# Performance work log

Hardware: AMD Instinct MI355X
Metric: run time of the kernel (lower is better)

Reference implementation:

```python
import jax, jax.numpy as jnp
import numpy as np

N_EMBD = 1024
N_HEAD = 16
HEAD_DIM = N_EMBD // N_HEAD
EPS = 1e-5


def setup_inputs() -> dict:
    key = jax.random.key(0)
    ks = jax.random.split(key, 12)
    C = N_EMBD
    s = lambda fan_in: 1.0 / np.sqrt(fan_in)
    return {
        "x": jax.random.normal(ks[0], (2, 2048, C), dtype=jnp.float32),
        "ln1_g": jnp.ones((C,), jnp.float32),
        "ln1_b": jnp.zeros((C,), jnp.float32),
        "w_attn": jax.random.normal(ks[1], (C, 3 * C), jnp.float32) * s(C),
        "b_attn": jnp.zeros((3 * C,), jnp.float32),
        "w_proj": jax.random.normal(ks[2], (C, C), jnp.float32) * s(C),
        "b_proj": jnp.zeros((C,), jnp.float32),
        "ln2_g": jnp.ones((C,), jnp.float32),
        "ln2_b": jnp.zeros((C,), jnp.float32),
        "w_fc": jax.random.normal(ks[3], (C, 4 * C), jnp.float32) * s(C),
        "b_fc": jnp.zeros((4 * C,), jnp.float32),
        "w_fc2": jax.random.normal(ks[4], (4 * C, C), jnp.float32) * s(4 * C),
        "b_fc2": jnp.zeros((C,), jnp.float32),
    }


def _layernorm(x, g, b):
    mu = jnp.mean(x, axis=-1, keepdims=True)
    var = jnp.mean(jnp.square(x - mu), axis=-1, keepdims=True)
    return (x - mu) * jax.lax.rsqrt(var + EPS) * g + b


def _attention(x, w_attn, b_attn, w_proj, b_proj):
    B, T, C = x.shape
    qkv = x @ w_attn + b_attn  # [B,T,3C]
    q, k, v = jnp.split(qkv, 3, axis=-1)
    # [B,H,T,D]
    reshape = lambda t: t.reshape(B, T, N_HEAD, HEAD_DIM).transpose(0, 2, 1, 3)
    q, k, v = reshape(q), reshape(k), reshape(v)
    scale = HEAD_DIM ** (-0.5)
    att = jnp.einsum("bhqd,bhkd->bhqk", q, k) * scale  # [B,H,T,T]
    mask = jnp.tril(jnp.ones((T, T), dtype=bool))
    att = jnp.where(mask, att, -jnp.inf)
    att = jax.nn.softmax(att, axis=-1)
    y = jnp.einsum("bhqk,bhkd->bhqd", att, v)
    y = y.transpose(0, 2, 1, 3).reshape(B, T, C)
    return y @ w_proj + b_proj


def _mlp(x, w_fc, b_fc, w_fc2, b_fc2):
    h = jax.nn.gelu(x @ w_fc + b_fc, approximate=False)  # nn.GELU default = exact erf
    return h @ w_fc2 + b_fc2


def reference(x, ln1_g, ln1_b, w_attn, b_attn, w_proj, b_proj,
              ln2_g, ln2_b, w_fc, b_fc, w_fc2, b_fc2):
    x = x + _attention(_layernorm(x, ln1_g, ln1_b), w_attn, b_attn, w_proj, b_proj)
    x = x + _mlp(_layernorm(x, ln2_g, ln2_b), w_fc, b_fc, w_fc2, b_fc2)
    return x
```

## Files before the change

kernel.cpp:

```cpp
#include <hip/hip_runtime.h>
#include <hip/hip_bf16.h>
#include <math.h>

typedef __attribute__((ext_vector_type(8))) __bf16 bf16x8;
typedef __attribute__((ext_vector_type(4))) float floatx4;
typedef __attribute__((ext_vector_type(8))) unsigned short ushort8;

#define C_EMBD 1024
#define T_SEQ 2048
#define NH 16
#define HD 64

static __device__ __forceinline__ unsigned short f2b(float f) {
  __hip_bfloat16 h = __float2bfloat16(f);
  unsigned short u;
  __builtin_memcpy(&u, &h, sizeof(u));
  return u;
}
static __device__ __forceinline__ float b2f(unsigned short u) {
  unsigned int b = ((unsigned int)u) << 16;
  float f;
  __builtin_memcpy(&f, &b, sizeof(f));
  return f;
}

static __device__ __forceinline__ void gload16(const void* g, void* l) {
  __builtin_amdgcn_global_load_lds(
      (__attribute__((address_space(1))) void*)(void*)g,
      (__attribute__((address_space(3))) void*)l, 16, 0, 0);
}

static __device__ __forceinline__ floatx4 mfma_bf16(bf16x8 a, bf16x8 b, floatx4 c) {
  return __builtin_amdgcn_mfma_f32_16x16x32_bf16(a, b, c, 0, 0, 0);
}

__global__ __launch_bounds__(256) void wtrans(const float* __restrict__ in,
                                              unsigned short* __restrict__ out,
                                              int K, int N) {
  __shared__ float t[32][33];
  int n0 = blockIdx.x * 32, k0 = blockIdx.y * 32;
  int tx = threadIdx.x & 31, ty = threadIdx.x >> 5;
#pragma unroll
  for (int i = 0; i < 4; i++)
    t[ty + i * 8][tx] = in[(size_t)(k0 + ty + i * 8) * N + n0 + tx];
  __syncthreads();
#pragma unroll
  for (int i = 0; i < 4; i++)
    out[(size_t)(n0 + ty + i * 8) * K + k0 + tx] = f2b(t[tx][ty + i * 8]);
}

__global__ __launch_bounds__(256) void ln_fwd(const float* __restrict__ x,
                                              const float* __restrict__ g,
                                              const float* __restrict__ bta,
                                              unsigned short* __restrict__ out) {
  int row = blockIdx.x;
  int t = threadIdx.x;
  const float4* xr = (const float4*)(x + (size_t)row * C_EMBD);
  float4 v = xr[t];
  float s = v.x + v.y + v.z + v.w;
  float ss = v.x * v.x + v.y * v.y + v.z * v.z + v.w * v.w;
#pragma unroll
  for (int m = 1; m < 64; m <<= 1) {
    s += __shfl_xor(s, m, 64);
    ss += __shfl_xor(ss, m, 64);
  }
  __shared__ float ps[8];
  int wv = t >> 6;
  if ((t & 63) == 0) { ps[wv] = s; ps[4 + wv] = ss; }
  __syncthreads();
  s = ps[0] + ps[1] + ps[2] + ps[3];
  ss = ps[4] + ps[5] + ps[6] + ps[7];
  float mu = s * (1.0f / C_EMBD);
  float var = ss * (1.0f / C_EMBD) - mu * mu;
  float rs = rsqrtf(var + 1e-5f);
  float4 gv = ((const float4*)g)[t];
  float4 bv = ((const float4*)bta)[t];
  ushort4 o;
  o.x = f2b((v.x - mu) * rs * gv.x + bv.x);
  o.y = f2b((v.y - mu) * rs * gv.y + bv.y);
  o.z = f2b((v.z - mu) * rs * gv.z + bv.z);
  o.w = f2b((v.w - mu) * rs * gv.w + bv.w);
  *(ushort4*)(out + (size_t)row * C_EMBD + t * 4) = o;
}

template <int EP, int MI>
__global__ __launch_bounds__(256) void gemm_bt(const unsigned short* __restrict__ A,
                                               const unsigned short* __restrict__ Bt,
                                               const float* __restrict__ bias,
                                               const float* __restrict__ res,
                                               void* __restrict__ outv,
                                               unsigned short* __restrict__ vt,
                                               int M, int N, int K) {
  __shared__ __align__(16) unsigned short As[MI * 32 * 32];
  __shared__ __align__(16) unsigned short Bs[128 * 32];
  const int tid = threadIdx.x;
  const int wv = tid >> 6, ln = tid & 63;
  const int quad = ln >> 4, l15 = ln & 15;
  const int wm = wv >> 1, wn = wv & 1;
  const int m0 = blockIdx.y * (MI * 32), n0 = blockIdx.x * 128;

  floatx4 acc[MI][4];
#pragma unroll
  for (int i = 0; i < MI; i++)
#pragma unroll
    for (int j = 0; j < 4; j++) acc[i][j] = (floatx4)0.0f;

  const int rowA = ln >> 2;
  const int koff = (ln & 3) * 8;

  for (int k0 = 0; k0 < K; k0 += 32) {
    if (k0) __syncthreads();
#pragma unroll
    for (int hh = 0; hh < MI / 2; ++hh) {
      int r = hh * 64 + wv * 16 + rowA;
      gload16(A + (size_t)(m0 + r) * K + k0 + koff, &As[(hh * 64 + wv * 16) * 32]);
    }
#pragma unroll
    for (int hh = 0; hh < 2; ++hh) {
      int r = hh * 64 + wv * 16 + rowA;
      gload16(Bt + (size_t)(n0 + r) * K + k0 + koff, &Bs[(hh * 64 + wv * 16) * 32]);
    }
    __syncthreads();
    bf16x8 af[MI], bfr[4];
#pragma unroll
    for (int mi = 0; mi < MI; mi++)
      af[mi] = *(const bf16x8*)&As[(wm * (MI * 16) + mi * 16 + l15) * 32 + quad * 8];
#pragma unroll
    for (int ni = 0; ni < 4; ni++)
      bfr[ni] = *(const bf16x8*)&Bs[(wn * 64 + ni * 16 + l15) * 32 + quad * 8];
#pragma unroll
    for (int mi = 0; mi < MI; mi++)
#pragma unroll
      for (int ni = 0; ni < 4; ni++)
        acc[mi][ni] = mfma_bf16(af[mi], bfr[ni], acc[mi][ni]);
  }

#pragma unroll
  for (int mi = 0; mi < MI; mi++) {
#pragma unroll
    for (int ni = 0; ni < 4; ni++) {
      int col = n0 + wn * 64 + ni * 16 + l15;
      int rowb = m0 + wm * (MI * 16) + mi * 16 + quad * 4;
      float bc = bias[col];
      if (EP == 1) {
#pragma unroll
        for (int r = 0; r < 4; r++) {
          size_t idx = (size_t)(rowb + r) * N + col;
          ((float*)outv)[idx] = acc[mi][ni][r] + bc + res[idx];
        }
      } else if (EP == 2) {
#pragma unroll
        for (int r = 0; r < 4; r++) {
          float v = acc[mi][ni][r] + bc;
          v = 0.5f * v * (1.0f + erff(v * 0.70710678118f));
          ((unsigned short*)outv)[(size_t)(rowb + r) * N + col] = f2b(v);
        }
      } else {
        if (col < 2048) {
#pragma unroll
          for (int r = 0; r < 4; r++)
            ((unsigned short*)outv)[(size_t)(rowb + r) * N + col] =
                f2b(acc[mi][ni][r] + bc);
        } else {
          int dall = col - 2048;
          int hh2 = dall >> 6, dd = dall & 63;
          int bq = rowb >> 11, t0 = rowb & 2047;
          __align__(8) unsigned short pk[4];
#pragma unroll
          for (int r = 0; r < 4; r++) pk[r] = f2b(acc[mi][ni][r] + bc);
          *(ushort4*)&vt[(size_t)((bq * NH + hh2) * HD + dd) * T_SEQ + t0] =
              *(const ushort4*)pk;
        }
      }
    }
  }
}

__global__ __launch_bounds__(256) void attn_fwd(const unsigned short* __restrict__ qkv,
                                                const unsigned short* __restrict__ vt,
                                                unsigned short* __restrict__ y) {
  __shared__ __align__(16) unsigned short Ks[64 * 64];
  __shared__ __align__(16) unsigned short Vs[64 * 64];
  __shared__ __align__(16) unsigned short Ps[4 * 16 * 72];
  const int tid = threadIdx.x;
  const int wv = tid >> 6, ln = tid & 63;
  const int quad = ln >> 4, l15 = ln & 15;
  const int pair = blockIdx.x, h = blockIdx.y, b = blockIdx.z;
  unsigned short* Pw = &Ps[wv * 16 * 72];

  const unsigned short* kbase = qkv + (size_t)b * T_SEQ * 3072 + 1024 + h * HD;
  const unsigned short* vbase = vt + (size_t)(b * NH + h) * HD * T_SEQ;

  int koffs[2], voffs[2], ldst[2];
#pragma unroll
  for (int g = 0; g < 2; g++) {
    int S = wv * 128 + g * 64 + ln;
    int r = S >> 3;
    int c = (S & 7) ^ (r & 7);
    koffs[g] = r * 3072 + c * 8;
    voffs[g] = r * T_SEQ + c * 8;
    ldst[g] = wv * 1024 + g * 512;
  }

  for (int ph = 0; ph < 2; ++ph) {
    const int qt = ph ? (31 - pair) : pair;
    const unsigned short* qp =
        qkv + (size_t)(b * T_SEQ + qt * 64 + wv * 16 + l15) * 3072 + h * HD;
    bf16x8 qf[2];
#pragma unroll
    for (int kc = 0; kc < 2; kc++) {
      ushort8 u = *(const ushort8*)(qp + kc * 32 + quad * 8);
      union { ushort8 u; bf16x8 v; } cv;
#pragma unroll
      for (int j = 0; j < 8; j++) cv.u[j] = f2b(b2f(u[j]) * 0.18033688f);
      qf[kc] = cv.v;
    }

    floatx4 o[4];
#pragma unroll
    for (int dt = 0; dt < 4; dt++) o[dt] = (floatx4)0.0f;
    float lacc = 0.0f;

    auto step = [&](int kt, bool diag) {
      __syncthreads();
#pragma unroll
      for (int g = 0; g < 2; g++) {
        gload16(kbase + (size_t)(kt * 64) * 3072 + koffs[g], &Ks[ldst[g]]);
        gload16(vbase + kt * 64 + voffs[g], &Vs[ldst[g]]);
      }
      __syncthreads();

      floatx4 s[4];
#pragma unroll
      for (int nt = 0; nt < 4; nt++) s[nt] = (floatx4)0.0f;
#pragma unroll
      for (int nt = 0; nt < 4; nt++)
#pragma unroll
        for (int kc = 0; kc < 2; kc++) {
          bf16x8 kf = *(const bf16x8*)
              &Ks[(nt * 16 + l15) * 64 + (((kc * 4 + quad) ^ (l15 & 7)) * 8)];
          s[nt] = mfma_bf16(kf, qf[kc], s[nt]);
        }

      float psum = 0.0f;
#pragma unroll
      for (int nt = 0; nt < 4; nt++) {
        __align__(8) unsigned short pk[4];
#pragma unroll
        for (int r = 0; r < 4; r++) {
          float sv = s[nt][r];
          if (diag && (nt * 16 + quad * 4 + r > wv * 16 + l15)) sv = -1e30f;
          float p = exp2f(sv - 12.0f);
          psum += p;
          pk[r] = f2b(p);
        }
        *(ushort4*)&Pw[l15 * 72 + nt * 16 + quad * 4] = *(const ushort4*)pk;
      }
      lacc += psum;

      bf16x8 pf0 = *(const bf16x8*)&Pw[l15 * 72 + quad * 8];
      bf16x8 pf1 = *(const bf16x8*)&Pw[l15 * 72 + 32 + quad * 8];
#pragma unroll
      for (int dt = 0; dt < 4; dt++) {
        bf16x8 vf0 = *(const bf16x8*)
            &Vs[(dt * 16 + l15) * 64 + ((quad ^ (l15 & 7)) * 8)];
        bf16x8 vf1 = *(const bf16x8*)
            &Vs[(dt * 16 + l15) * 64 + (((4 + quad) ^ (l15 & 7)) * 8)];
        o[dt] = mfma_bf16(vf0, pf0, o[dt]);
        o[dt] = mfma_bf16(vf1, pf1, o[dt]);
      }
    };

    for (int kt = 0; kt < qt; ++kt) step(kt, false);
    step(qt, true);

    lacc += __shfl_xor(lacc, 16, 64);
    lacc += __shfl_xor(lacc, 32, 64);
    float rinv = 1.0f / lacc;
#pragma unroll
    for (int dt = 0; dt < 4; dt++) {
      __align__(8) unsigned short ov[4];
#pragma unroll
      for (int r = 0; r < 4; r++) ov[r] = f2b(o[dt][r] * rinv);
      *(ushort4*)&y[(size_t)(b * T_SEQ + qt * 64 + wv * 16 + l15) * C_EMBD +
                    h * HD + dt * 16 + quad * 4] = *(const ushort4*)ov;
    }
  }
}

extern "C" void kernel_launch(void* const* d_in, const int* in_sizes, int n_in,
                              void* d_out, int out_size, void* d_ws, size_t ws_size,
                              hipStream_t stream) {
  (void)in_sizes; (void)n_in; (void)out_size; (void)ws_size;
  const float* x      = (const float*)d_in[0];
  const float* ln1_g  = (const float*)d_in[1];
  const float* ln1_b  = (const float*)d_in[2];
  const float* w_attn = (const float*)d_in[3];
  const float* b_attn = (const float*)d_in[4];
  const float* w_proj = (const float*)d_in[5];
  const float* b_proj = (const float*)d_in[6];
  const float* ln2_g  = (const float*)d_in[7];
  const float* ln2_b  = (const float*)d_in[8];
  const float* w_fc   = (const float*)d_in[9];
  const float* b_fc   = (const float*)d_in[10];
  const float* w_fc2  = (const float*)d_in[11];
  const float* b_fc2  = (const float*)d_in[12];
  float* out = (float*)d_out;

  char* ws = (char*)d_ws;
  unsigned short* wat  = (unsigned short*)ws; ws += (size_t)3072 * 1024 * 2;
  unsigned short* wpt  = (unsigned short*)ws; ws += (size_t)1024 * 1024 * 2;
  unsigned short* wft  = (unsigned short*)ws; ws += (size_t)4096 * 1024 * 2;
  unsigned short* wf2t = (unsigned short*)ws; ws += (size_t)1024 * 4096 * 2;
  unsigned short* xn   = (unsigned short*)ws; ws += (size_t)4096 * 1024 * 2;
  unsigned short* qkv  = (unsigned short*)ws; ws += (size_t)4096 * 3072 * 2;
  unsigned short* yat  = (unsigned short*)ws; ws += (size_t)4096 * 1024 * 2;
  unsigned short* hbuf = (unsigned short*)ws; ws += (size_t)4096 * 4096 * 2;
  unsigned short* vt = hbuf;

  wtrans<<<dim3(3072 / 32, 1024 / 32), 256, 0, stream>>>(w_attn, wat, 1024, 3072);
  wtrans<<<dim3(1024 / 32, 1024 / 32), 256, 0, stream>>>(w_proj, wpt, 1024, 1024);
  wtrans<<<dim3(4096 / 32, 1024 / 32), 256, 0, stream>>>(w_fc, wft, 1024, 4096);
  wtrans<<<dim3(1024 / 32, 4096 / 32), 256, 0, stream>>>(w_fc2, wf2t, 4096, 1024);

  ln_fwd<<<4096, 256, 0, stream>>>(x, ln1_g, ln1_b, xn);
  gemm_bt<3, 4><<<dim3(24, 32), 256, 0, stream>>>(
      xn, wat, b_attn, nullptr, qkv, vt, 4096, 3072, 1024);
  attn_fwd<<<dim3(16, NH, 2), 256, 0, stream>>>(qkv, vt, yat);
  gemm_bt<1, 2><<<dim3(8, 64), 256, 0, stream>>>(
      yat, wpt, b_proj, x, out, nullptr, 4096, 1024, 1024);
  ln_fwd<<<4096, 256, 0, stream>>>(out, ln2_g, ln2_b, xn);
  gemm_bt<2, 4><<<dim3(32, 32), 256, 0, stream>>>(
      xn, wft, b_fc, nullptr, hbuf, nullptr, 4096, 4096, 1024);
  gemm_bt<1, 2><<<dim3(8, 64), 256, 0, stream>>>(
      hbuf, wf2t, b_fc2, out, out, nullptr, 4096, 1024, 4096);
}
```

Baseline: 384.5 us.

## Split-K the residual GEMMs with atomic accumulation and swizzle LDS reads

After: 414.6 us. +7.8%, slower.

```diff
diff --git a/kernel.cpp b/kernel.cpp
--- a/kernel.cpp
+++ b/kernel.cpp
@@ -87,7 +87,6 @@
 __global__ __launch_bounds__(256) void gemm_bt(const unsigned short* __restrict__ A,
                                                const unsigned short* __restrict__ Bt,
                                                const float* __restrict__ bias,
-                                               const float* __restrict__ res,
                                                void* __restrict__ outv,
                                                unsigned short* __restrict__ vt,
                                                int M, int N, int K) {
@@ -98,6 +97,9 @@
   const int quad = ln >> 4, l15 = ln & 15;
   const int wm = wv >> 1, wn = wv & 1;
   const int m0 = blockIdx.y * (MI * 32), n0 = blockIdx.x * 128;
+  const int kz = blockIdx.z;
+  const int Kp = K / gridDim.z;
+  const int kbeg = kz * Kp, kend = kbeg + Kp;
 
   floatx4 acc[MI][4];
 #pragma unroll
@@ -106,10 +108,11 @@
     for (int j = 0; j < 4; j++) acc[i][j] = (floatx4)0.0f;
 
   const int rowA = ln >> 2;
-  const int koff = (ln & 3) * 8;
-
-  for (int k0 = 0; k0 < K; k0 += 32) {
-    if (k0) __syncthreads();
+  const int koff = (((ln & 3) ^ ((ln >> 3) & 3)) * 8);
+  const int swz = (l15 >> 1) & 3;
+
+  for (int k0 = kbeg; k0 < kend; k0 += 32) {
+    if (k0 != kbeg) __syncthreads();
 #pragma unroll
     for (int hh = 0; hh < MI / 2; ++hh) {
       int r = hh * 64 + wv * 16 + rowA;
@@ -124,10 +127,12 @@
     bf16x8 af[MI], bfr[4];
 #pragma unroll
     for (int mi = 0; mi < MI; mi++)
-      af[mi] = *(const bf16x8*)&As[(wm * (MI * 16) + mi * 16 + l15) * 32 + quad * 8];
+      af[mi] = *(const bf16x8*)
+          &As[(wm * (MI * 16) + mi * 16 + l15) * 32 + (quad ^ swz) * 8];
 #pragma unroll
     for (int ni = 0; ni < 4; ni++)
-      bfr[ni] = *(const bf16x8*)&Bs[(wn * 64 + ni * 16 + l15) * 32 + quad * 8];
+      bfr[ni] = *(const bf16x8*)
+          &Bs[(wn * 64 + ni * 16 + l15) * 32 + (quad ^ swz) * 8];
 #pragma unroll
     for (int mi = 0; mi < MI; mi++)
 #pragma unroll
@@ -143,10 +148,11 @@
       int rowb = m0 + wm * (MI * 16) + mi * 16 + quad * 4;
       float bc = bias[col];
       if (EP == 1) {
+        float badd = (kz == 0) ? bc : 0.0f;
 #pragma unroll
         for (int r = 0; r < 4; r++) {
           size_t idx = (size_t)(rowb + r) * N + col;
-          ((float*)outv)[idx] = acc[mi][ni][r] + bc + res[idx];
+          atomicAdd(&((float*)outv)[idx], acc[mi][ni][r] + badd);
         }
       } else if (EP == 2) {
 #pragma unroll
@@ -318,6 +324,8 @@
   unsigned short* hbuf = (unsigned short*)ws; ws += (size_t)4096 * 4096 * 2;
   unsigned short* vt = hbuf;
 
+  hipMemcpyAsync(out, x, (size_t)4096 * 1024 * 4, hipMemcpyDeviceToDevice, stream);
+
   wtrans<<<dim3(3072 / 32, 1024 / 32), 256, 0, stream>>>(w_attn, wat, 1024, 3072);
   wtrans<<<dim3(1024 / 32, 1024 / 32), 256, 0, stream>>>(w_proj, wpt, 1024, 1024);
   wtrans<<<dim3(4096 / 32, 1024 / 32), 256, 0, stream>>>(w_fc, wft, 1024, 4096);
@@ -325,13 +333,13 @@
 
   ln_fwd<<<4096, 256, 0, stream>>>(x, ln1_g, ln1_b, xn);
   gemm_bt<3, 4><<<dim3(24, 32), 256, 0, stream>>>(
-      xn, wat, b_attn, nullptr, qkv, vt, 4096, 3072, 1024);
+      xn, wat, b_attn, qkv, vt, 4096, 3072, 1024);
   attn_fwd<<<dim3(16, NH, 2), 256, 0, stream>>>(qkv, vt, yat);
-  gemm_bt<1, 2><<<dim3(8, 64), 256, 0, stream>>>(
-      yat, wpt, b_proj, x, out, nullptr, 4096, 1024, 1024);
+  gemm_bt<1, 2><<<dim3(8, 64, 2), 256, 0, stream>>>(
+      yat, wpt, b_proj, out, nullptr, 4096, 1024, 1024);
   ln_fwd<<<4096, 256, 0, stream>>>(out, ln2_g, ln2_b, xn);
   gemm_bt<2, 4><<<dim3(32, 32), 256, 0, stream>>>(
-      xn, wft, b_fc, nullptr, hbuf, nullptr, 4096, 4096, 1024);
-  gemm_bt<1, 2><<<dim3(8, 64), 256, 0, stream>>>(
-      hbuf, wf2t, b_fc2, out, out, nullptr, 4096, 1024, 4096);
-}
+      xn, wft, b_fc, hbuf, nullptr, 4096, 4096, 1024);
+  gemm_bt<1, 2><<<dim3(8, 64, 2), 256, 0, stream>>>(
+      hbuf, wf2t, b_fc2, out, nullptr, 4096, 1024, 4096);
+}
```

## Add XOR-swizzled LDS and a double-buffered 512-thread GEMM for N=1024 projections

Applied to the files above, without the earlier changes.

New measurement: 387.2 us. About the same (+0.7%).

```diff
diff --git a/kernel.cpp b/kernel.cpp
--- a/kernel.cpp
+++ b/kernel.cpp
@@ -83,72 +83,62 @@
   *(ushort4*)(out + (size_t)row * C_EMBD + t * 4) = o;
 }
 
-template <int EP, int MI>
+template <int EP>
 __global__ __launch_bounds__(256) void gemm_bt(const unsigned short* __restrict__ A,
                                                const unsigned short* __restrict__ Bt,
                                                const float* __restrict__ bias,
-                                               const float* __restrict__ res,
                                                void* __restrict__ outv,
                                                unsigned short* __restrict__ vt,
                                                int M, int N, int K) {
-  __shared__ __align__(16) unsigned short As[MI * 32 * 32];
+  __shared__ __align__(16) unsigned short As[128 * 32];
   __shared__ __align__(16) unsigned short Bs[128 * 32];
   const int tid = threadIdx.x;
   const int wv = tid >> 6, ln = tid & 63;
   const int quad = ln >> 4, l15 = ln & 15;
   const int wm = wv >> 1, wn = wv & 1;
-  const int m0 = blockIdx.y * (MI * 32), n0 = blockIdx.x * 128;
-
-  floatx4 acc[MI][4];
-#pragma unroll
-  for (int i = 0; i < MI; i++)
+  const int m0 = blockIdx.y * 128, n0 = blockIdx.x * 128;
+
+  floatx4 acc[4][4];
+#pragma unroll
+  for (int i = 0; i < 4; i++)
 #pragma unroll
     for (int j = 0; j < 4; j++) acc[i][j] = (floatx4)0.0f;
 
   const int rowA = ln >> 2;
-  const int koff = (ln & 3) * 8;
+  const int koff = (((ln & 3) ^ ((ln >> 3) & 3)) * 8);
+  const int swz = (l15 >> 1) & 3;
 
   for (int k0 = 0; k0 < K; k0 += 32) {
     if (k0) __syncthreads();
 #pragma unroll
-    for (int hh = 0; hh < MI / 2; ++hh) {
+    for (int hh = 0; hh < 2; ++hh) {
       int r = hh * 64 + wv * 16 + rowA;
       gload16(A + (size_t)(m0 + r) * K + k0 + koff, &As[(hh * 64 + wv * 16) * 32]);
-    }
-#pragma unroll
-    for (int hh = 0; hh < 2; ++hh) {
-      int r = hh * 64 + wv * 16 + rowA;
       gload16(Bt + (size_t)(n0 + r) * K + k0 + koff, &Bs[(hh * 64 + wv * 16) * 32]);
     }
     __syncthreads();
-    bf16x8 af[MI], bfr[4];
-#pragma unroll
-    for (int mi = 0; mi < MI; mi++)
-      af[mi] = *(const bf16x8*)&As[(wm * (MI * 16) + mi * 16 + l15) * 32 + quad * 8];
+    bf16x8 af[4], bfr[4];
+#pragma unroll
+    for (int mi = 0; mi < 4; mi++)
+      af[mi] = *(const bf16x8*)&As[(wm * 64 + mi * 16 + l15) * 32 + (quad ^ swz) * 8];
 #pragma unroll
     for (int ni = 0; ni < 4; ni++)
-      bfr[ni] = *(const bf16x8*)&Bs[(wn * 64 + ni * 16 + l15) * 32 + quad * 8];
-#pragma unroll
-    for (int mi = 0; mi < MI; mi++)
+      bfr[ni] = *(const bf16x8*)&Bs[(wn * 64 + ni * 16 + l15) * 32 + (quad ^ swz) * 8];
+#pragma unroll
+    for (int mi = 0; mi < 4; mi++)
 #pragma unroll
       for (int ni = 0; ni < 4; ni++)
         acc[mi][ni] = mfma_bf16(af[mi], bfr[ni], acc[mi][ni]);
   }
 
 #pragma unroll
-  for (int mi = 0; mi < MI; mi++) {
+  for (int mi = 0; mi < 4; mi++) {
 #pragma unroll
     for (int ni = 0; ni < 4; ni++) {
       int col = n0 + wn * 64 + ni * 16 + l15;
-      int rowb = m0 + wm * (MI * 16) + mi * 16 + quad * 4;
+      int rowb = m0 + wm * 64 + mi * 16 + quad * 4;
       float bc = bias[col];
-      if (EP == 1) {
-#pragma unroll
-        for (int r = 0; r < 4; r++) {
-          size_t idx = (size_t)(rowb + r) * N + col;
-          ((float*)outv)[idx] = acc[mi][ni][r] + bc + res[idx];
-        }
-      } else if (EP == 2) {
+      if (EP == 2) {
 #pragma unroll
         for (int r = 0; r < 4; r++) {
           float v = acc[mi][ni][r] + bc;
@@ -171,6 +161,81 @@
           *(ushort4*)&vt[(size_t)((bq * NH + hh2) * HD + dd) * T_SEQ + t0] =
               *(const ushort4*)pk;
         }
+      }
+    }
+  }
+}
+
+__global__ __launch_bounds__(512) void gemm_skinny(const unsigned short* __restrict__ A,
+                                                   const unsigned short* __restrict__ Bt,
+                                                   const float* __restrict__ bias,
+                                                   const float* res, float* out,
+                                                   int M, int N, int K) {
+  __shared__ __align__(16) unsigned short As[2][128 * 32];
+  __shared__ __align__(16) unsigned short Bs[2][128 * 32];
+  const int tid = threadIdx.x;
+  const int wv = tid >> 6, ln = tid & 63;
+  const int quad = ln >> 4, l15 = ln & 15;
+  const int wm = wv >> 1, wn = wv & 1;
+  const int m0 = blockIdx.y * 128, n0 = blockIdx.x * 128;
+
+  floatx4 acc[2][4];
+#pragma unroll
+  for (int i = 0; i < 2; i++)
+#pragma unroll
+    for (int j = 0; j < 4; j++) acc[i][j] = (floatx4)0.0f;
+
+  const int rowA = ln >> 2;
+  const int koff = (((ln & 3) ^ ((ln >> 3) & 3)) * 8);
+  const int swz = (l15 >> 1) & 3;
+
+  const unsigned short* aseg = A + (size_t)(m0 + wv * 16 + rowA) * K + koff;
+  const unsigned short* bseg = Bt + (size_t)(n0 + wv * 16 + rowA) * K + koff;
+  const int ldsOff = (wv * 16) * 32;
+
+  const int nIter = K >> 5;
+  gload16(aseg, &As[0][ldsOff]);
+  gload16(bseg, &Bs[0][ldsOff]);
+
+  for (int it = 0; it < nIter; ++it) {
+    if (it + 1 < nIter) {
+      int k1 = (it + 1) << 5;
+      int nb = (it + 1) & 1;
+      gload16(aseg + k1, &As[nb][ldsOff]);
+      gload16(bseg + k1, &Bs[nb][ldsOff]);
+      asm volatile("s_waitcnt vmcnt(2)" ::: "memory");
+    } else {
+      asm volatile("s_waitcnt vmcnt(0)" ::: "memory");
+    }
+    asm volatile("s_barrier" ::: "memory");
+    const unsigned short* as = As[it & 1];
+    const unsigned short* bs = Bs[it & 1];
+    bf16x8 af[2], bfr[4];
+#pragma unroll
+    for (int mi = 0; mi < 2; mi++)
+      af[mi] = *(const bf16x8*)&as[(wm * 32 + mi * 16 + l15) * 32 + (quad ^ swz) * 8];
+#pragma unroll
+    for (int ni = 0; ni < 4; ni++)
+      bfr[ni] = *(const bf16x8*)&bs[(wn * 64 + ni * 16 + l15) * 32 + (quad ^ swz) * 8];
+#pragma unroll
+    for (int mi = 0; mi < 2; mi++)
+#pragma unroll
+      for (int ni = 0; ni < 4; ni++)
+        acc[mi][ni] = mfma_bf16(af[mi], bfr[ni], acc[mi][ni]);
+    asm volatile("s_barrier" ::: "memory");
+  }
+
+#pragma unroll
+  for (int mi = 0; mi < 2; mi++) {
+#pragma unroll
+    for (int ni = 0; ni < 4; ni++) {
+      int col = n0 + wn * 64 + ni * 16 + l15;
+      int rowb = m0 + wm * 32 + mi * 16 + quad * 4;
+      float bc = bias[col];
+#pragma unroll
+      for (int r = 0; r < 4; r++) {
+        size_t idx = (size_t)(rowb + r) * N + col;
+        out[idx] = acc[mi][ni][r] + bc + res[idx];
       }
     }
   }
@@ -324,14 +389,14 @@
   wtrans<<<dim3(1024 / 32, 4096 / 32), 256, 0, stream>>>(w_fc2, wf2t, 4096, 1024);
 
   ln_fwd<<<4096, 256, 0, stream>>>(x, ln1_g, ln1_b, xn);
-  gemm_bt<3, 4><<<dim3(24, 32), 256, 0, stream>>>(
-      xn, wat, b_attn, nullptr, qkv, vt, 4096, 3072, 1024);
+  gemm_bt<3><<<dim3(24, 32), 256, 0, stream>>>(
+      xn, wat, b_attn, qkv, vt, 4096, 3072, 1024);
   attn_fwd<<<dim3(16, NH, 2), 256, 0, stream>>>(qkv, vt, yat);
-  gemm_bt<1, 2><<<dim3(8, 64), 256, 0, stream>>>(
-      yat, wpt, b_proj, x, out, nullptr, 4096, 1024, 1024);
+  gemm_skinny<<<dim3(8, 32), 512, 0, stream>>>(
+      yat, wpt, b_proj, x, out, 4096, 1024, 1024);
   ln_fwd<<<4096, 256, 0, stream>>>(out, ln2_g, ln2_b, xn);
-  gemm_bt<2, 4><<<dim3(32, 32), 256, 0, stream>>>(
-      xn, wft, b_fc, nullptr, hbuf, nullptr, 4096, 4096, 1024);
-  gemm_bt<1, 2><<<dim3(8, 64), 256, 0, stream>>>(
-      hbuf, wf2t, b_fc2, out, out, nullptr, 4096, 1024, 4096);
-}
+  gemm_bt<2><<<dim3(32, 32), 256, 0, stream>>>(
+      xn, wft, b_fc, hbuf, nullptr, 4096, 4096, 1024);
+  gemm_skinny<<<dim3(8, 32), 512, 0, stream>>>(
+      hbuf, wf2t, b_fc2, out, out, 4096, 1024, 4096);
+}
```
